# Kernel optimization log

Hardware: AMD Instinct MI355X
Metric: run time of the kernel (lower is better)

Reference implementation:

```python
import jax, jax.numpy as jnp
import numpy as np

IN_CH, H0, H1, OUT_CH = 6, 128, 256, 256
EPS = 1e-5

def _layernorm(x, g, b):
    mu = jnp.mean(x, axis=-1, keepdims=True)
    var = jnp.mean(jnp.square(x - mu), axis=-1, keepdims=True)
    return (x - mu) * jax.lax.rsqrt(var + EPS) * g + b

def setup_inputs() -> dict:
    key = jax.random.key(0)
    ks = jax.random.split(key, 12)
    B, N, C = 8, 65536, 1024
    inp = {
        "point_patches": jax.random.normal(ks[0], (B, N, IN_CH), jnp.float32),
        "nn_idx": jax.random.randint(ks[1], (B, N), 0, C, jnp.int64),
        "center_number": C,
        # conv1: Linear(6,128) -> LN(128) -> GELU -> Linear(128,128)
        "w1": jax.random.normal(ks[2], (IN_CH, H0), jnp.float32) / np.sqrt(IN_CH),
        "b1": jnp.zeros((H0,), jnp.float32),
        "g1": jnp.ones((H0,), jnp.float32),
        "beta1": jnp.zeros((H0,), jnp.float32),
        "w2": jax.random.normal(ks[3], (H0, H0), jnp.float32) / np.sqrt(H0),
        "b2": jnp.zeros((H0,), jnp.float32),
        # conv2: Linear(256,256) -> LN(256) -> GELU -> Linear(256,256)
        "w3": jax.random.normal(ks[4], (2 * H0, H1), jnp.float32) / np.sqrt(2 * H0),
        "b3": jnp.zeros((H1,), jnp.float32),
        "g2": jnp.ones((H1,), jnp.float32),
        "beta2": jnp.zeros((H1,), jnp.float32),
        "w4": jax.random.normal(ks[5], (H1, OUT_CH), jnp.float32) / np.sqrt(H1),
        "b4": jnp.zeros((OUT_CH,), jnp.float32),
    }
    return inp

def _scatter_max_zeros(x, nn_idx, center_number):
    # torch.scatter_reduce(zeros, 1, idx, x, 'max') with include_self=True:
    # segment max clamped from below at 0; empty centers stay 0.
    B = x.shape[0]
    y = jnp.zeros((B, center_number, x.shape[-1]), x.dtype)
    return y.at[jnp.arange(B)[:, None], nn_idx].max(x)

def reference(point_patches, nn_idx, center_number, w1, b1, g1, beta1, w2, b2, w3, b3, g2, beta2, w4, b4):
    # conv1 MLP
    h = point_patches @ w1 + b1
    h = jax.nn.gelu(_layernorm(h, g1, beta1), approximate=False)
    x = h @ w2 + b2                                   # [B, N, H0]
    # scatter-max to centers, gather back per point
    y = _scatter_max_zeros(x, nn_idx, center_number)  # [B, C, H0]
    x_max = jnp.take_along_axis(y, nn_idx[:, :, None], axis=1)  # [B, N, H0]
    x = jnp.concatenate([x_max, x], axis=-1)          # [B, N, 2*H0]
    # conv2 MLP
    h = x @ w3 + b3
    h = jax.nn.gelu(_layernorm(h, g2, beta2), approximate=False)
    x = h @ w4 + b4                                   # [B, N, OUT]
    return _scatter_max_zeros(x, nn_idx, center_number)  # [B, C, OUT]
```

## Files before the change

kernel.cpp:

```cpp
#include <hip/hip_runtime.h>

typedef short short8 __attribute__((ext_vector_type(8)));
typedef float f32x4 __attribute__((ext_vector_type(4)));

#define DEVI __device__ __forceinline__

constexpr int BATCH = 8;
constexpr int NPTS  = 65536;
constexpr int CIN   = 6;
constexpr int H0    = 128;
constexpr int H1    = 256;
constexpr int NCTR  = 1024;
constexpr int MB    = 64;
constexpr int NCHUNK = 8;
constexpr int CHSZ  = NPTS / NCHUNK;

constexpr int A1S = 136;
constexpr int A2S = 264;

constexpr int CAP1 = 8;
constexpr int CAP2 = 8;

constexpr size_t Y_BYTES  = (size_t)BATCH * NCTR * H0 * 4;
constexpr size_t W2T_OFF  = Y_BYTES;
constexpr size_t W3T_OFF  = W2T_OFF + (size_t)H0 * H0 * 2;
constexpr size_t W4T_OFF  = W3T_OFF + (size_t)H1 * H1 * 2;
constexpr size_t SORT_OFF = W4T_OFF + (size_t)H1 * H1 * 2;
constexpr size_t CH_OFF   = SORT_OFF + (size_t)BATCH * NPTS * 4;
constexpr size_t CB_OFF   = CH_OFF + (size_t)BATCH * NCHUNK * NCTR * 4;
constexpr size_t YQ_OFF   = CB_OFF + (size_t)BATCH * NCHUNK * NCTR * 4;
constexpr size_t WS_NEED  = YQ_OFF + (size_t)BATCH * NCTR * H0 * 2;
constexpr size_t XQ_OFF   = WS_NEED;
constexpr size_t WS_XQ    = XQ_OFF + (size_t)BATCH * NPTS * H0 * 2;

DEVI unsigned short f2bf(float f) {
    unsigned u = __float_as_uint(f);
    u += 0x7fffu + ((u >> 16) & 1u);
    return (unsigned short)(u >> 16);
}
DEVI float gelu(float x) {
    const float x3 = x * x * x;
    const float u = fmaf(x3, -0.07135481283f, -1.5957691216f * x);
    return x * __builtin_amdgcn_rcpf(1.f + __expf(u));
}

DEVI void conv1_tile(int tid, const float* s_pts, const float* s_w1,
                     const float* s_b1, const float* s_g1, const float* s_be1,
                     unsigned short* a1)
{
    const int p = tid >> 2, sub = tid & 3;
    float pt[CIN];
#pragma unroll
    for (int k = 0; k < CIN; ++k) pt[k] = s_pts[p * CIN + k];
    float h[32];
#pragma unroll
    for (int j = 0; j < 32; ++j) {
        const int c = (j << 2) + sub;
        float a = s_b1[c];
#pragma unroll
        for (int k = 0; k < CIN; ++k) a = fmaf(pt[k], s_w1[k * H0 + c], a);
        h[j] = a;
    }
    float s = 0.f, s2 = 0.f;
#pragma unroll
    for (int j = 0; j < 32; ++j) { s += h[j]; s2 = fmaf(h[j], h[j], s2); }
    s  += __shfl_xor(s, 1);  s  += __shfl_xor(s, 2);
    s2 += __shfl_xor(s2, 1); s2 += __shfl_xor(s2, 2);
    const float mean = s * (1.f / H0);
    const float rstd = rsqrtf(s2 * (1.f / H0) - mean * mean + 1e-5f);
#pragma unroll
    for (int j = 0; j < 32; ++j) {
        const int c = (j << 2) + sub;
        float v = fmaf((h[j] - mean) * rstd, s_g1[c], s_be1[c]);
        a1[p * A1S + c] = f2bf(gelu(v));
    }
}

DEVI void gemm2(int lane, int wave, const unsigned short* a1,
                const unsigned short* __restrict__ w2T, f32x4 (&acc)[4][2])
{
    const int q = lane >> 4, colw = lane & 15, n0 = wave * 32;
#pragma unroll
    for (int ks = 0; ks < 4; ++ks) {
        short8 af[4], bfr[2];
#pragma unroll
        for (int mt = 0; mt < 4; ++mt)
            af[mt] = *(const short8*)&a1[(mt * 16 + colw) * A1S + ks * 32 + q * 8];
#pragma unroll
        for (int nt = 0; nt < 2; ++nt)
            bfr[nt] = *(const short8*)&w2T[(n0 + nt * 16 + colw) * H0 + ks * 32 + q * 8];
#pragma unroll
        for (int mt = 0; mt < 4; ++mt)
#pragma unroll
            for (int nt = 0; nt < 2; ++nt)
                acc[mt][nt] = __builtin_amdgcn_mfma_f32_16x16x32_bf16(
                    af[mt], bfr[nt], acc[mt][nt], 0, 0, 0);
    }
}

DEVI void stage_sorted(int tid, int b, int P0, const int* __restrict__ sorted,
                       const float* __restrict__ pts, float* s_pts, int* s_idx)
{
    if (tid < 64) {
        const int val = sorted[P0 + tid];
        const int pid = val & 0xFFFF;
        s_idx[tid] = (val >> 16) & (NCTR - 1);
        const float* prow = &pts[((size_t)(b << 16) + pid) * CIN];
#pragma unroll
        for (int k = 0; k < CIN; ++k) s_pts[tid * CIN + k] = prow[k];
    }
}

DEVI void slot_scan(int tid, const int* s_idx, int* s_slot, int* s_slotc, int* s_nslot, int cap)
{
    int f = 0;
    if (tid < MB) {
        f = (tid > 0 && s_idx[tid] != s_idx[tid - 1]) ? 1 : 0;
        s_slot[tid] = f;
    }
    __syncthreads();
#pragma unroll
    for (int off = 1; off < MB; off <<= 1) {
        int t = 0;
        if (tid < MB && tid >= off) t = s_slot[tid - off];
        __syncthreads();
        if (tid < MB) s_slot[tid] += t;
        __syncthreads();
    }
    if (tid < MB) {
        const int s = s_slot[tid];
        if ((f || tid == 0) && s < cap) s_slotc[s] = s_idx[tid];
        if (tid == MB - 1) *s_nslot = (s + 1 < cap) ? (s + 1) : cap;
    }
    __syncthreads();
}

__global__ __launch_bounds__(256) void k_prep(
    const float* __restrict__ w2, const float* __restrict__ w3,
    const float* __restrict__ w4,
    unsigned short* __restrict__ w2T, unsigned short* __restrict__ w3T,
    unsigned short* __restrict__ w4T)
{
    int t = blockIdx.x * 256 + threadIdx.x;
    if (t < H0 * H0) {
        int n = t >> 7, k = t & 127;
        w2T[t] = f2bf(w2[k * H0 + n]);
    }
    int t3 = t - H0 * H0;
    if (t3 >= 0 && t3 < H1 * H1) {
        int n = t3 >> 8, k = t3 & 255;
        w3T[t3] = f2bf(w3[k * H1 + n]);
    }
    int t4 = t - (H0 * H0 + H1 * H1);
    if (t4 >= 0 && t4 < H1 * H1) {
        int n = t4 >> 8, k = t4 & 255;
        w4T[t4] = f2bf(w4[k * H1 + n]);
    }
}

__global__ __launch_bounds__(256) void k_yq(const float* __restrict__ y,
                                            unsigned short* __restrict__ yq)
{
    const int i = blockIdx.x * 256 + threadIdx.x;
    const float4 v = *(const float4*)&y[(size_t)i * 4];
    uint2 pk;
    pk.x = (unsigned)f2bf(v.x) | ((unsigned)f2bf(v.y) << 16);
    pk.y = (unsigned)f2bf(v.z) | ((unsigned)f2bf(v.w) << 16);
    *(uint2*)&yq[(size_t)i * 4] = pk;
}

__global__ __launch_bounds__(256) void k_hist(const int* __restrict__ nn,
                                              int* __restrict__ ch)
{
    __shared__ int lh[NCTR];
    const int tid = threadIdx.x;
    const int b = blockIdx.x >> 3, k = blockIdx.x & 7;
    const int base = (b << 16) + k * CHSZ;
    for (int c = tid; c < NCTR; c += 256) lh[c] = 0;
    __syncthreads();
    for (int i = tid; i < CHSZ; i += 256)
        atomicAdd(&lh[nn[base + i] & (NCTR - 1)], 1);
    __syncthreads();
    for (int c = tid; c < NCTR; c += 256) ch[(blockIdx.x << 10) + c] = lh[c];
}

__global__ __launch_bounds__(256) void k_scan(const int* __restrict__ ch,
                                              int* __restrict__ cb)
{
    __shared__ int part[256];
    const int tid = threadIdx.x;
    const int b = tid >> 5, t = tid & 31;
    const int c0 = t * 32;
    int tot = 0;
    for (int c = c0; c < c0 + 32; ++c)
        for (int k = 0; k < NCHUNK; ++k)
            tot += ch[((b * NCHUNK + k) << 10) + c];
    part[tid] = tot;
    __syncthreads();
    if (t == 0) {
        int run = 0;
        for (int i = 0; i < 32; ++i) { const int v = part[(b << 5) + i]; part[(b << 5) + i] = run; run += v; }
    }
    __syncthreads();
    int run = part[tid];
    for (int c = c0; c < c0 + 32; ++c)
        for (int k = 0; k < NCHUNK; ++k) {
            const int idx = ((b * NCHUNK + k) << 10) + c;
            cb[idx] = run; run += ch[idx];
        }
}

__global__ __launch_bounds__(256) void k_scatter(const int* __restrict__ nn,
                                                 const int* __restrict__ cb,
                                                 int* __restrict__ sorted)
{
    __shared__ int cur[NCTR];
    const int tid = threadIdx.x;
    const int b = blockIdx.x >> 3, k = blockIdx.x & 7;
    const int base = (b << 16) + k * CHSZ;
    for (int c = tid; c < NCTR; c += 256) cur[c] = cb[(blockIdx.x << 10) + c];
    __syncthreads();
    for (int i = tid; i < CHSZ; i += 256) {
        const int c = nn[base + i] & (NCTR - 1);
        const int pos = atomicAdd(&cur[c], 1);
        if ((unsigned)pos < (unsigned)NPTS)
            sorted[(b << 16) + pos] = (k * CHSZ + i) | (c << 16);
    }
}

template <bool XQ>
__global__ __launch_bounds__(256) void k_phase1(
    const int* __restrict__ sorted, const float* __restrict__ pts,
    const float* __restrict__ w1, const float* __restrict__ b1,
    const float* __restrict__ g1, const float* __restrict__ be1,
    const unsigned short* __restrict__ w2T, const float* __restrict__ b2,
    float* __restrict__ y, unsigned short* __restrict__ xq)
{
    __shared__ __align__(16) float s_pts[MB * CIN];
    __shared__ int   s_idx[MB], s_slot[MB], s_slotc[CAP1], s_nslot;
    __shared__ float s_w1[CIN * H0];
    __shared__ float s_b1[H0], s_g1[H0], s_be1[H0];
    __shared__ __align__(16) unsigned short a1[MB * A1S];
    __shared__ int   red1[CAP1 * H0];

    const int tid = threadIdx.x;
    const int P0  = blockIdx.x * MB;
    const int b   = P0 >> 16;
    const int lane = tid & 63, wave = tid >> 6;
    const int q = lane >> 4, colw = lane & 15, n0 = wave * 32;

    float b2reg[2];
#pragma unroll
    for (int nt = 0; nt < 2; ++nt) b2reg[nt] = b2[n0 + nt * 16 + colw];

    stage_sorted(tid, b, P0, sorted, pts, s_pts, s_idx);
    for (int i = tid; i < CIN * H0; i += 256) s_w1[i] = w1[i];
    if (tid < H0) { s_b1[tid] = b1[tid]; s_g1[tid] = g1[tid]; s_be1[tid] = be1[tid]; }
    for (int i = tid; i < CAP1 * H0; i += 256) red1[i] = 0;
    __syncthreads();

    conv1_tile(tid, s_pts, s_w1, s_b1, s_g1, s_be1, a1);
    slot_scan(tid, s_idx, s_slot, s_slotc, &s_nslot, CAP1);

    f32x4 acc[4][2] = {};
    gemm2(lane, wave, a1, w2T, acc);
    if (XQ) __syncthreads();

    int* yi = (int*)y;
    {
        float vm[2] = {-3.4e38f, -3.4e38f};
        int cur = s_slot[q * 4], curc = s_idx[q * 4];
#pragma unroll
        for (int mt = 0; mt < 4; ++mt)
#pragma unroll
            for (int r = 0; r < 4; ++r) {
                const int row = mt * 16 + q * 4 + r;
                const int s = s_slot[row];
                if (s != cur) {
#pragma unroll
                    for (int nt = 0; nt < 2; ++nt) {
                        if (vm[nt] > 0.f) {
                            const int col = n0 + nt * 16 + colw;
                            if (cur < CAP1) atomicMax(&red1[cur * H0 + col], __float_as_int(vm[nt]));
                            else atomicMax(&yi[(((b << 10) + curc) << 7) + col], __float_as_int(vm[nt]));
                        }
                        vm[nt] = -3.4e38f;
                    }
                    cur = s; curc = s_idx[row];
                }
#pragma unroll
                for (int nt = 0; nt < 2; ++nt) {
                    const float v = acc[mt][nt][r] + b2reg[nt];
                    if (XQ) a1[row * A1S + n0 + nt * 16 + colw] = f2bf(v);
                    vm[nt] = fmaxf(vm[nt], v);
                }
            }
#pragma unroll
        for (int nt = 0; nt < 2; ++nt)
            if (vm[nt] > 0.f) {
                const int col = n0 + nt * 16 + colw;
                if (cur < CAP1) atomicMax(&red1[cur * H0 + col], __float_as_int(vm[nt]));
                else atomicMax(&yi[(((b << 10) + curc) << 7) + col], __float_as_int(vm[nt]));
            }
    }
    __syncthreads();
    const int nsc = s_nslot;
    for (int i = tid; i < nsc * H0; i += 256) {
        const int v = red1[i];
        if (v > 0)
            atomicMax(&yi[(((b << 10) + s_slotc[i >> 7]) << 7) + (i & 127)], v);
    }
    if (XQ) {
        for (int i = tid; i < MB * (H0 / 8); i += 256) {
            const int row = i >> 4, u = (i & 15) * 8;
            *(short8*)&xq[((size_t)P0 + row) * H0 + u] = *(const short8*)&a1[row * A1S + u];
        }
    }
}

__global__ __launch_bounds__(256) void k_phase2x(
    const int* __restrict__ sorted, const unsigned short* __restrict__ xq,
    const unsigned short* __restrict__ yq,
    const unsigned short* __restrict__ w3T, const float* __restrict__ b3,
    const float* __restrict__ g2, const float* __restrict__ be2,
    const unsigned short* __restrict__ w4T, const float* __restrict__ b4,
    float* __restrict__ outp)
{
    __shared__ int   s_idx[MB], s_slot[MB], s_slotc[CAP2], s_nslot;
    __shared__ __align__(16) unsigned short a2[MB * A2S];
    __shared__ float2 s_stats[MB * 4];
    __shared__ float2 s_rowstat[MB];

    const int tid = threadIdx.x;
    const int P0  = blockIdx.x * MB;
    const int b   = P0 >> 16;
    const int lane = tid & 63, wave = tid >> 6;
    const int q = lane >> 4, colw = lane & 15;
    const int n0 = wave * 64;

    const int rowp = tid >> 2, sub = tid & 3;
    const int sval = sorted[P0 + rowp];
    const int cp = (sval >> 16) & (NCTR - 1);
    const unsigned short* xsrc = &xq[((size_t)P0 + rowp) * H0 + sub * 32];
    short8 xv0 = *(const short8*)(xsrc);
    short8 xv1 = *(const short8*)(xsrc + 8);
    short8 xv2 = *(const short8*)(xsrc + 16);
    short8 xv3 = *(const short8*)(xsrc + 24);
    const unsigned short* ysrc = &yq[((size_t)((b << 10) + cp)) * H0 + sub * 32];
    short8 yv0 = *(const short8*)(ysrc);
    short8 yv1 = *(const short8*)(ysrc + 8);
    short8 yv2 = *(const short8*)(ysrc + 16);
    short8 yv3 = *(const short8*)(ysrc + 24);

    float b3r[4], g2r[4], be2r[4], b4r[4];
#pragma unroll
    for (int nt = 0; nt < 4; ++nt) {
        const int col = n0 + nt * 16 + colw;
        b3r[nt] = b3[col]; g2r[nt] = g2[col]; be2r[nt] = be2[col]; b4r[nt] = b4[col];
    }

    if (tid < 64) s_idx[tid] = (sorted[P0 + tid] >> 16) & (NCTR - 1);

    {
        unsigned short* dx = &a2[rowp * A2S + H0 + sub * 32];
        *(short8*)(dx)      = xv0;
        *(short8*)(dx + 8)  = xv1;
        *(short8*)(dx + 16) = xv2;
        *(short8*)(dx + 24) = xv3;
        unsigned short* dy = &a2[rowp * A2S + sub * 32];
        *(short8*)(dy)      = yv0;
        *(short8*)(dy + 8)  = yv1;
        *(short8*)(dy + 16) = yv2;
        *(short8*)(dy + 24) = yv3;
    }
    __syncthreads();
    slot_scan(tid, s_idx, s_slot, s_slotc, &s_nslot, CAP2);

    f32x4 acc3[4][4] = {};
#pragma unroll
    for (int ks = 0; ks < 8; ++ks) {
        short8 af[4], bfr[4];
#pragma unroll
        for (int mt = 0; mt < 4; ++mt)
            af[mt] = *(const short8*)&a2[(mt * 16 + colw) * A2S + ks * 32 + q * 8];
#pragma unroll
        for (int nt = 0; nt < 4; ++nt)
            bfr[nt] = *(const short8*)&w3T[(n0 + nt * 16 + colw) * H1 + ks * 32 + q * 8];
#pragma unroll
        for (int mt = 0; mt < 4; ++mt)
#pragma unroll
            for (int nt = 0; nt < 4; ++nt)
                acc3[mt][nt] = __builtin_amdgcn_mfma_f32_16x16x32_bf16(
                    af[mt], bfr[nt], acc3[mt][nt], 0, 0, 0);
    }

#pragma unroll
    for (int mt = 0; mt < 4; ++mt)
#pragma unroll
        for (int nt = 0; nt < 4; ++nt)
#pragma unroll
            for (int r = 0; r < 4; ++r)
                acc3[mt][nt][r] += b3r[nt];

#pragma unroll
    for (int mt = 0; mt < 4; ++mt)
#pragma unroll
        for (int r = 0; r < 4; ++r) {
            float s = 0.f, s2 = 0.f;
#pragma unroll
            for (int nt = 0; nt < 4; ++nt) {
                float v = acc3[mt][nt][r];
                s += v; s2 = fmaf(v, v, s2);
            }
            s  += __shfl_xor(s, 1);  s  += __shfl_xor(s, 2);
            s  += __shfl_xor(s, 4);  s  += __shfl_xor(s, 8);
            s2 += __shfl_xor(s2, 1); s2 += __shfl_xor(s2, 2);
            s2 += __shfl_xor(s2, 4); s2 += __shfl_xor(s2, 8);
            if (colw == 0)
                s_stats[(mt * 16 + q * 4 + r) * 4 + wave] = make_float2(s, s2);
        }
    __syncthreads();
    if (tid < MB) {
        float S = 0.f, S2 = 0.f;
#pragma unroll
        for (int w = 0; w < 4; ++w) { float2 t = s_stats[tid * 4 + w]; S += t.x; S2 += t.y; }
        const float mean = S * (1.f / H1);
        const float rstd = rsqrtf(S2 * (1.f / H1) - mean * mean + 1e-5f);
        s_rowstat[tid] = make_float2(mean, rstd);
    }
    __syncthreads();

#pragma unroll
    for (int mt = 0; mt < 4; ++mt)
#pragma unroll
        for (int r = 0; r < 4; ++r) {
            const int row = mt * 16 + q * 4 + r;
            const float2 ms = s_rowstat[row];
#pragma unroll
            for (int nt = 0; nt < 4; ++nt) {
                float v = (acc3[mt][nt][r] - ms.x) * ms.y;
                v = fmaf(v, g2r[nt], be2r[nt]);
                a2[row * A2S + n0 + nt * 16 + colw] = f2bf(gelu(v));
            }
        }
    __syncthreads();

    f32x4 acc4[4][4] = {};
#pragma unroll
    for (int ks = 0; ks < 8; ++ks) {
        short8 af[4], bfr[4];
#pragma unroll
        for (int mt = 0; mt < 4; ++mt)
            af[mt] = *(const short8*)&a2[(mt * 16 + colw) * A2S + ks * 32 + q * 8];
#pragma unroll
        for (int nt = 0; nt < 4; ++nt)
            bfr[nt] = *(const short8*)&w4T[(n0 + nt * 16 + colw) * H1 + ks * 32 + q * 8];
#pragma unroll
        for (int mt = 0; mt < 4; ++mt)
#pragma unroll
            for (int nt = 0; nt < 4; ++nt)
                acc4[mt][nt] = __builtin_amdgcn_mfma_f32_16x16x32_bf16(
                    af[mt], bfr[nt], acc4[mt][nt], 0, 0, 0);
    }
    __syncthreads();

    int* red = (int*)a2;
    for (int i = tid; i < CAP2 * H1; i += 256) red[i] = 0;
    __syncthreads();

    int* outi = (int*)outp;
    {
        float vm[4] = {-3.4e38f, -3.4e38f, -3.4e38f, -3.4e38f};
        int cur = s_slot[q * 4], curc = s_idx[q * 4];
#pragma unroll
        for (int mt = 0; mt < 4; ++mt)
#pragma unroll
            for (int r = 0; r < 4; ++r) {
                const int row = mt * 16 + q * 4 + r;
                const int s = s_slot[row];
                if (s != cur) {
#pragma unroll
                    for (int nt = 0; nt < 4; ++nt) {
                        if (vm[nt] > 0.f) {
                            const int col = n0 + nt * 16 + colw;
                            if (cur < CAP2) atomicMax(&red[cur * H1 + col], __float_as_int(vm[nt]));
                            else atomicMax(&outi[(((size_t)(b << 10) + curc) << 8) + col], __float_as_int(vm[nt]));
                        }
                        vm[nt] = -3.4e38f;
                    }
                    cur = s; curc = s_idx[row];
                }
#pragma unroll
                for (int nt = 0; nt < 4; ++nt)
                    vm[nt] = fmaxf(vm[nt], acc4[mt][nt][r] + b4r[nt]);
            }
#pragma unroll
        for (int nt = 0; nt < 4; ++nt)
            if (vm[nt] > 0.f) {
                const int col = n0 + nt * 16 + colw;
                if (cur < CAP2) atomicMax(&red[cur * H1 + col], __float_as_int(vm[nt]));
                else atomicMax(&outi[(((size_t)(b << 10) + curc) << 8) + col], __float_as_int(vm[nt]));
            }
    }
    __syncthreads();
    const int nsc = s_nslot;
    for (int i = tid; i < nsc * H1; i += 256) {
        const int v = red[i];
        if (v > 0)
            atomicMax(&outi[(((size_t)(b << 10) + s_slotc[i >> 8]) << 8) + (i & 255)], v);
    }
}

__global__ __launch_bounds__(256) void k_phase2r(
    const int* __restrict__ sorted, const float* __restrict__ pts,
    const float* __restrict__ w1, const float* __restrict__ b1,
    const float* __restrict__ g1, const float* __restrict__ be1,
    const unsigned short* __restrict__ w2T, const float* __restrict__ b2,
    const float* __restrict__ y,
    const unsigned short* __restrict__ w3T, const float* __restrict__ b3,
    const float* __restrict__ g2, const float* __restrict__ be2,
    const unsigned short* __restrict__ w4T, const float* __restrict__ b4,
    float* __restrict__ outp)
{
    __shared__ __align__(16) float s_pts[MB * CIN];
    __shared__ int   s_idx[MB], s_slot[MB], s_slotc[CAP2], s_nslot;
    __shared__ float s_w1[CIN * H0];
    __shared__ float s_b1[H0], s_g1[H0], s_be1[H0], s_b2[H0];
    __shared__ float s_b3[H1], s_g2[H1], s_be2[H1], s_b4[H1];
    __shared__ union __align__(16) {
        unsigned short a1[MB * A1S];
        struct { float2 stats[MB * 4]; float2 rowstat[MB]; } ln;
        int red[CAP2 * H1];
    } u1;
    __shared__ __align__(16) unsigned short a2[MB * A2S];

    const int tid = threadIdx.x;
    const int P0  = blockIdx.x * MB;
    const int b   = P0 >> 16;

    stage_sorted(tid, b, P0, sorted, pts, s_pts, s_idx);
    for (int i = tid; i < CIN * H0; i += 256) s_w1[i] = w1[i];
    if (tid < H0) { s_b1[tid] = b1[tid]; s_g1[tid] = g1[tid]; s_be1[tid] = be1[tid]; s_b2[tid] = b2[tid]; }
    if (tid < H1) { s_b3[tid] = b3[tid]; s_g2[tid] = g2[tid]; s_be2[tid] = be2[tid]; s_b4[tid] = b4[tid]; }
    __syncthreads();

    conv1_tile(tid, s_pts, s_w1, s_b1, s_g1, s_be1, u1.a1);
    slot_scan(tid, s_idx, s_slot, s_slotc, &s_nslot, CAP2);

    f32x4 acc2[4][2] = {};
    const int lane = tid & 63, wave = tid >> 6;
    gemm2(lane, wave, u1.a1, w2T, acc2);

    const int q = lane >> 4, colw = lane & 15;
    {
        const int n0 = wave * 32;
#pragma unroll
        for (int mt = 0; mt < 4; ++mt)
#pragma unroll
            for (int nt = 0; nt < 2; ++nt)
#pragma unroll
                for (int r = 0; r < 4; ++r) {
                    const int row = mt * 16 + q * 4 + r;
                    const int col = n0 + nt * 16 + colw;
                    a2[row * A2S + H0 + col] = f2bf(acc2[mt][nt][r] + s_b2[col]);
                }
    }
    {
        const int p = tid >> 2, sub = tid & 3;
        const float* yrow = y + ((size_t)((b << 10) + s_idx[p])) * H0;
#pragma unroll
        for (int j4 = 0; j4 < 8; ++j4) {
            const int c = sub * 32 + j4 * 4;
            float4 v = *(const float4*)&yrow[c];
            uint2 pk;
            pk.x = (unsigned)f2bf(v.x) | ((unsigned)f2bf(v.y) << 16);
            pk.y = (unsigned)f2bf(v.z) | ((unsigned)f2bf(v.w) << 16);
            *(uint2*)&a2[p * A2S + c] = pk;
        }
    }
    __syncthreads();

    f32x4 acc3[4][4] = {};
    const int n0 = wave * 64;
#pragma unroll
    for (int ks = 0; ks < 8; ++ks) {
        short8 af[4], bfr[4];
#pragma unroll
        for (int mt = 0; mt < 4; ++mt)
            af[mt] = *(const short8*)&a2[(mt * 16 + colw) * A2S + ks * 32 + q * 8];
#pragma unroll
        for (int nt = 0; nt < 4; ++nt)
            bfr[nt] = *(const short8*)&w3T[(n0 + nt * 16 + colw) * H1 + ks * 32 + q * 8];
#pragma unroll
        for (int mt = 0; mt < 4; ++mt)
#pragma unroll
            for (int nt = 0; nt < 4; ++nt)
                acc3[mt][nt] = __builtin_amdgcn_mfma_f32_16x16x32_bf16(
                    af[mt], bfr[nt], acc3[mt][nt], 0, 0, 0);
    }

#pragma unroll
    for (int mt = 0; mt < 4; ++mt)
#pragma unroll
        for (int nt = 0; nt < 4; ++nt)
#pragma unroll
            for (int r = 0; r < 4; ++r)
                acc3[mt][nt][r] += s_b3[n0 + nt * 16 + colw];

#pragma unroll
    for (int mt = 0; mt < 4; ++mt)
#pragma unroll
        for (int r = 0; r < 4; ++r) {
            float s = 0.f, s2 = 0.f;
#pragma unroll
            for (int nt = 0; nt < 4; ++nt) {
                float v = acc3[mt][nt][r];
                s += v; s2 = fmaf(v, v, s2);
            }
            s  += __shfl_xor(s, 1);  s  += __shfl_xor(s, 2);
            s  += __shfl_xor(s, 4);  s  += __shfl_xor(s, 8);
            s2 += __shfl_xor(s2, 1); s2 += __shfl_xor(s2, 2);
            s2 += __shfl_xor(s2, 4); s2 += __shfl_xor(s2, 8);
            if (colw == 0)
                u1.ln.stats[(mt * 16 + q * 4 + r) * 4 + wave] = make_float2(s, s2);
        }
    __syncthreads();
    if (tid < MB) {
        float S = 0.f, S2 = 0.f;
#pragma unroll
        for (int w = 0; w < 4; ++w) { float2 t = u1.ln.stats[tid * 4 + w]; S += t.x; S2 += t.y; }
        const float mean = S * (1.f / H1);
        const float rstd = rsqrtf(S2 * (1.f / H1) - mean * mean + 1e-5f);
        u1.ln.rowstat[tid] = make_float2(mean, rstd);
    }
    __syncthreads();

#pragma unroll
    for (int mt = 0; mt < 4; ++mt)
#pragma unroll
        for (int r = 0; r < 4; ++r) {
            const int row = mt * 16 + q * 4 + r;
            const float2 ms = u1.ln.rowstat[row];
#pragma unroll
            for (int nt = 0; nt < 4; ++nt) {
                const int col = n0 + nt * 16 + colw;
                float v = (acc3[mt][nt][r] - ms.x) * ms.y;
                v = fmaf(v, s_g2[col], s_be2[col]);
                a2[row * A2S + col] = f2bf(gelu(v));
            }
        }
    __syncthreads();

    for (int i = tid; i < CAP2 * H1; i += 256) u1.red[i] = 0;

    f32x4 acc4[4][4] = {};
#pragma unroll
    for (int ks = 0; ks < 8; ++ks) {
        short8 af[4], bfr[4];
#pragma unroll
        for (int mt = 0; mt < 4; ++mt)
            af[mt] = *(const short8*)&a2[(mt * 16 + colw) * A2S + ks * 32 + q * 8];
#pragma unroll
        for (int nt = 0; nt < 4; ++nt)
            bfr[nt] = *(const short8*)&w4T[(n0 + nt * 16 + colw) * H1 + ks * 32 + q * 8];
#pragma unroll
        for (int mt = 0; mt < 4; ++mt)
#pragma unroll
            for (int nt = 0; nt < 4; ++nt)
                acc4[mt][nt] = __builtin_amdgcn_mfma_f32_16x16x32_bf16(
                    af[mt], bfr[nt], acc4[mt][nt], 0, 0, 0);
    }
    __syncthreads();

    int* outi = (int*)outp;
#pragma unroll
    for (int mt = 0; mt < 4; ++mt)
#pragma unroll
        for (int nt = 0; nt < 4; ++nt)
#pragma unroll
            for (int r = 0; r < 4; ++r) {
                const int row = mt * 16 + q * 4 + r;
                const int col = n0 + nt * 16 + colw;
                const float v = acc4[mt][nt][r] + s_b4[col];
                if (v > 0.f) {
                    const int s = s_slot[row];
                    if (s < CAP2)
                        atomicMax(&u1.red[s * H1 + col], __float_as_int(v));
                    else
                        atomicMax(&outi[(((size_t)(b << 10) + s_idx[row]) << 8) + col],
                                  __float_as_int(v));
                }
            }
    __syncthreads();
    const int nsc = s_nslot;
    for (int i = tid; i < nsc * H1; i += 256) {
        const int v = u1.red[i];
        if (v > 0)
            atomicMax(&outi[(((size_t)(b << 10) + s_slotc[i >> 8]) << 8) + (i & 255)], v);
    }
}

extern "C" void kernel_launch(void* const* d_in, const int* in_sizes, int n_in,
                              void* d_out, int out_size, void* d_ws, size_t ws_size,
                              hipStream_t stream)
{
    const float* pts = (const float*)d_in[0];
    const int*   nn  = (const int*)d_in[1];
    const float* w1  = (const float*)d_in[3];
    const float* b1  = (const float*)d_in[4];
    const float* g1  = (const float*)d_in[5];
    const float* be1 = (const float*)d_in[6];
    const float* w2  = (const float*)d_in[7];
    const float* b2  = (const float*)d_in[8];
    const float* w3  = (const float*)d_in[9];
    const float* b3  = (const float*)d_in[10];
    const float* g2  = (const float*)d_in[11];
    const float* be2 = (const float*)d_in[12];
    const float* w4  = (const float*)d_in[13];
    const float* b4  = (const float*)d_in[14];

    if (ws_size < WS_NEED) return;

    char* ws = (char*)d_ws;
    float*          y      = (float*)(ws);
    unsigned short* w2T    = (unsigned short*)(ws + W2T_OFF);
    unsigned short* w3T    = (unsigned short*)(ws + W3T_OFF);
    unsigned short* w4T    = (unsigned short*)(ws + W4T_OFF);
    int*            sorted = (int*)(ws + SORT_OFF);
    int*            ch     = (int*)(ws + CH_OFF);
    int*            cb     = (int*)(ws + CB_OFF);
    unsigned short* yq     = (unsigned short*)(ws + YQ_OFF);
    unsigned short* xq     = (unsigned short*)(ws + XQ_OFF);
    float* outp = (float*)d_out;
    const bool have_xq = ws_size >= WS_XQ;

    hipMemsetAsync(y, 0, Y_BYTES, stream);
    hipMemsetAsync(outp, 0, (size_t)out_size * sizeof(float), stream);

    k_prep<<<576, 256, 0, stream>>>(w2, w3, w4, w2T, w3T, w4T);
    k_hist<<<BATCH * NCHUNK, 256, 0, stream>>>(nn, ch);
    k_scan<<<1, 256, 0, stream>>>(ch, cb);
    k_scatter<<<BATCH * NCHUNK, 256, 0, stream>>>(nn, cb, sorted);

    const int nblk = BATCH * NPTS / MB;
    if (have_xq) {
        k_phase1<true><<<nblk, 256, 0, stream>>>(sorted, pts, w1, b1, g1, be1, w2T, b2, y, xq);
        k_yq<<<BATCH * NCTR * H0 / 4 / 256, 256, 0, stream>>>(y, yq);
        k_phase2x<<<nblk, 256, 0, stream>>>(sorted, xq, yq, w3T, b3, g2, be2, w4T, b4, outp);
    } else {
        k_phase1<false><<<nblk, 256, 0, stream>>>(sorted, pts, w1, b1, g1, be1, w2T, b2, y, nullptr);
        k_phase2r<<<nblk, 256, 0, stream>>>(sorted, pts, w1, b1, g1, be1, w2T, b2, y,
                                            w3T, b3, g2, be2, w4T, b4, outp);
    }
}
```

Before: 531.1 us.

## Precompute nonempty-center ranks in scan, prefetch weight fragments, raise occupancy bounds

The scan kernel now also writes an exclusive prefix count of non-empty centers per batch. Phase kernels use it to compute each row's reduction slot directly instead of running a per-block slot scan. The weight B-fragments for the GEMMs are software-pipelined, with the next k-step loaded before the current MFMAs issue, and launch bounds request 4 blocks per SM. This cuts block-level serial scan work and hides global weight-load latency, at the cost of more registers and possible spills under the tighter bound.

```diff
diff --git a/kernel.cpp b/kernel.cpp
--- a/kernel.cpp
+++ b/kernel.cpp
@@ -28,7 +28,8 @@
 constexpr size_t SORT_OFF = W4T_OFF + (size_t)H1 * H1 * 2;
 constexpr size_t CH_OFF   = SORT_OFF + (size_t)BATCH * NPTS * 4;
 constexpr size_t CB_OFF   = CH_OFF + (size_t)BATCH * NCHUNK * NCTR * 4;
-constexpr size_t YQ_OFF   = CB_OFF + (size_t)BATCH * NCHUNK * NCTR * 4;
+constexpr size_t NZR_OFF  = CB_OFF + (size_t)BATCH * NCHUNK * NCTR * 4;
+constexpr size_t YQ_OFF   = NZR_OFF + (size_t)BATCH * NCTR * 4;
 constexpr size_t WS_NEED  = YQ_OFF + (size_t)BATCH * NCTR * H0 * 2;
 constexpr size_t XQ_OFF   = WS_NEED;
 constexpr size_t WS_XQ    = XQ_OFF + (size_t)BATCH * NPTS * H0 * 2;
@@ -185,29 +186,40 @@
 }
 
 __global__ __launch_bounds__(256) void k_scan(const int* __restrict__ ch,
-                                              int* __restrict__ cb)
-{
-    __shared__ int part[256];
+                                              int* __restrict__ cb,
+                                              int* __restrict__ nzr)
+{
+    __shared__ int part[256], partz[256];
     const int tid = threadIdx.x;
     const int b = tid >> 5, t = tid & 31;
     const int c0 = t * 32;
-    int tot = 0;
-    for (int c = c0; c < c0 + 32; ++c)
+    int tot = 0, totz = 0;
+    for (int c = c0; c < c0 + 32; ++c) {
+        int cnt = 0;
         for (int k = 0; k < NCHUNK; ++k)
-            tot += ch[((b * NCHUNK + k) << 10) + c];
-    part[tid] = tot;
+            cnt += ch[((b * NCHUNK + k) << 10) + c];
+        tot += cnt; totz += (cnt > 0);
+    }
+    part[tid] = tot; partz[tid] = totz;
     __syncthreads();
     if (t == 0) {
-        int run = 0;
-        for (int i = 0; i < 32; ++i) { const int v = part[(b << 5) + i]; part[(b << 5) + i] = run; run += v; }
-    }
-    __syncthreads();
-    int run = part[tid];
-    for (int c = c0; c < c0 + 32; ++c)
+        int run = 0, runz = 0;
+        for (int i = 0; i < 32; ++i) {
+            const int v  = part[(b << 5) + i];  part[(b << 5) + i]  = run;  run  += v;
+            const int vz = partz[(b << 5) + i]; partz[(b << 5) + i] = runz; runz += vz;
+        }
+    }
+    __syncthreads();
+    int run = part[tid], runz = partz[tid];
+    for (int c = c0; c < c0 + 32; ++c) {
+        int cnt = 0;
         for (int k = 0; k < NCHUNK; ++k) {
             const int idx = ((b * NCHUNK + k) << 10) + c;
-            cb[idx] = run; run += ch[idx];
-        }
+            cb[idx] = run; run += ch[idx]; cnt += ch[idx];
+        }
+        nzr[(b << 10) + c] = runz;
+        runz += (cnt > 0);
+    }
 }
 
 __global__ __launch_bounds__(256) void k_scatter(const int* __restrict__ nn,
@@ -229,8 +241,9 @@
 }
 
 template <bool XQ>
-__global__ __launch_bounds__(256) void k_phase1(
+__global__ __launch_bounds__(256, 4) void k_phase1(
     const int* __restrict__ sorted, const float* __restrict__ pts,
+    const int* __restrict__ nzr,
     const float* __restrict__ w1, const float* __restrict__ b1,
     const float* __restrict__ g1, const float* __restrict__ be1,
     const unsigned short* __restrict__ w2T, const float* __restrict__ b2,
@@ -252,18 +265,57 @@
     float b2reg[2];
 #pragma unroll
     for (int nt = 0; nt < 2; ++nt) b2reg[nt] = b2[n0 + nt * 16 + colw];
-
-    stage_sorted(tid, b, P0, sorted, pts, s_pts, s_idx);
+    short8 bnx[2];
+#pragma unroll
+    for (int nt = 0; nt < 2; ++nt)
+        bnx[nt] = *(const short8*)&w2T[(n0 + nt * 16 + colw) * H0 + q * 8];
+
+    if (tid < 64) {
+        const int val = sorted[P0 + tid];
+        const int pid = val & 0xFFFF;
+        const int c   = (val >> 16) & (NCTR - 1);
+        const int c0v = (sorted[P0] >> 16) & (NCTR - 1);
+        s_idx[tid] = c;
+        const int sl = nzr[(b << 10) + c] - nzr[(b << 10) + c0v];
+        s_slot[tid] = sl;
+        if (tid == 63) s_nslot = (sl + 1 < CAP1) ? (sl + 1) : CAP1;
+        const float* prow = &pts[((size_t)(b << 16) + pid) * CIN];
+#pragma unroll
+        for (int k = 0; k < CIN; ++k) s_pts[tid * CIN + k] = prow[k];
+    }
     for (int i = tid; i < CIN * H0; i += 256) s_w1[i] = w1[i];
     if (tid < H0) { s_b1[tid] = b1[tid]; s_g1[tid] = g1[tid]; s_be1[tid] = be1[tid]; }
     for (int i = tid; i < CAP1 * H0; i += 256) red1[i] = 0;
     __syncthreads();
 
+    if (tid < 64) {
+        const int sl = s_slot[tid];
+        if (sl < CAP1 && (tid == 0 || s_idx[tid] != s_idx[tid - 1]))
+            s_slotc[sl] = s_idx[tid];
+    }
     conv1_tile(tid, s_pts, s_w1, s_b1, s_g1, s_be1, a1);
-    slot_scan(tid, s_idx, s_slot, s_slotc, &s_nslot, CAP1);
+    __syncthreads();
 
     f32x4 acc[4][2] = {};
-    gemm2(lane, wave, a1, w2T, acc);
+#pragma unroll
+    for (int ks = 0; ks < 4; ++ks) {
+        short8 bcur[2] = { bnx[0], bnx[1] };
+        if (ks < 3) {
+#pragma unroll
+            for (int nt = 0; nt < 2; ++nt)
+                bnx[nt] = *(const short8*)&w2T[(n0 + nt * 16 + colw) * H0 + (ks + 1) * 32 + q * 8];
+        }
+        short8 af[4];
+#pragma unroll
+        for (int mt = 0; mt < 4; ++mt)
+            af[mt] = *(const short8*)&a1[(mt * 16 + colw) * A1S + ks * 32 + q * 8];
+#pragma unroll
+        for (int mt = 0; mt < 4; ++mt)
+#pragma unroll
+            for (int nt = 0; nt < 2; ++nt)
+                acc[mt][nt] = __builtin_amdgcn_mfma_f32_16x16x32_bf16(
+                    af[mt], bcur[nt], acc[mt][nt], 0, 0, 0);
+    }
     if (XQ) __syncthreads();
 
     int* yi = (int*)y;
@@ -318,9 +370,9 @@
     }
 }
 
-__global__ __launch_bounds__(256) void k_phase2x(
+__global__ __launch_bounds__(256, 4) void k_phase2x(
     const int* __restrict__ sorted, const unsigned short* __restrict__ xq,
-    const unsigned short* __restrict__ yq,
+    const unsigned short* __restrict__ yq, const int* __restrict__ nzr,
     const unsigned short* __restrict__ w3T, const float* __restrict__ b3,
     const float* __restrict__ g2, const float* __restrict__ be2,
     const unsigned short* __restrict__ w4T, const float* __restrict__ b4,
@@ -358,9 +410,19 @@
         const int col = n0 + nt * 16 + colw;
         b3r[nt] = b3[col]; g2r[nt] = g2[col]; be2r[nt] = be2[col]; b4r[nt] = b4[col];
     }
-
-    if (tid < 64) s_idx[tid] = (sorted[P0 + tid] >> 16) & (NCTR - 1);
-
+    short8 bnx[4];
+#pragma unroll
+    for (int nt = 0; nt < 4; ++nt)
+        bnx[nt] = *(const short8*)&w3T[(n0 + nt * 16 + colw) * H1 + q * 8];
+
+    if (tid < 64) {
+        const int c   = (sorted[P0 + tid] >> 16) & (NCTR - 1);
+        const int c0v = (sorted[P0] >> 16) & (NCTR - 1);
+        s_idx[tid] = c;
+        const int sl = nzr[(b << 10) + c] - nzr[(b << 10) + c0v];
+        s_slot[tid] = sl;
+        if (tid == 63) s_nslot = (sl + 1 < CAP2) ? (sl + 1) : CAP2;
+    }
     {
         unsigned short* dx = &a2[rowp * A2S + H0 + sub * 32];
         *(short8*)(dx)      = xv0;
@@ -374,24 +436,32 @@
         *(short8*)(dy + 24) = yv3;
     }
     __syncthreads();
-    slot_scan(tid, s_idx, s_slot, s_slotc, &s_nslot, CAP2);
+
+    if (tid < 64) {
+        const int sl = s_slot[tid];
+        if (sl < CAP2 && (tid == 0 || s_idx[tid] != s_idx[tid - 1]))
+            s_slotc[sl] = s_idx[tid];
+    }
 
     f32x4 acc3[4][4] = {};
 #pragma unroll
     for (int ks = 0; ks < 8; ++ks) {
-        short8 af[4], bfr[4];
+        short8 bcur[4] = { bnx[0], bnx[1], bnx[2], bnx[3] };
+        if (ks < 7) {
+#pragma unroll
+            for (int nt = 0; nt < 4; ++nt)
+                bnx[nt] = *(const short8*)&w3T[(n0 + nt * 16 + colw) * H1 + (ks + 1) * 32 + q * 8];
+        }
+        short8 af[4];
 #pragma unroll
         for (int mt = 0; mt < 4; ++mt)
             af[mt] = *(const short8*)&a2[(mt * 16 + colw) * A2S + ks * 32 + q * 8];
-#pragma unroll
-        for (int nt = 0; nt < 4; ++nt)
-            bfr[nt] = *(const short8*)&w3T[(n0 + nt * 16 + colw) * H1 + ks * 32 + q * 8];
 #pragma unroll
         for (int mt = 0; mt < 4; ++mt)
 #pragma unroll
             for (int nt = 0; nt < 4; ++nt)
                 acc3[mt][nt] = __builtin_amdgcn_mfma_f32_16x16x32_bf16(
-                    af[mt], bfr[nt], acc3[mt][nt], 0, 0, 0);
+                    af[mt], bcur[nt], acc3[mt][nt], 0, 0, 0);
     }
 
 #pragma unroll
@@ -443,24 +513,31 @@
                 a2[row * A2S + n0 + nt * 16 + colw] = f2bf(gelu(v));
             }
         }
+    short8 b4x[4];
+#pragma unroll
+    for (int nt = 0; nt < 4; ++nt)
+        b4x[nt] = *(const short8*)&w4T[(n0 + nt * 16 + colw) * H1 + q * 8];
     __syncthreads();
 
     f32x4 acc4[4][4] = {};
 #pragma unroll
     for (int ks = 0; ks < 8; ++ks) {
-        short8 af[4], bfr[4];
+        short8 bcur[4] = { b4x[0], b4x[1], b4x[2], b4x[3] };
+        if (ks < 7) {
+#pragma unroll
+            for (int nt = 0; nt < 4; ++nt)
+                b4x[nt] = *(const short8*)&w4T[(n0 + nt * 16 + colw) * H1 + (ks + 1) * 32 + q * 8];
+        }
+        short8 af[4];
 #pragma unroll
         for (int mt = 0; mt < 4; ++mt)
             af[mt] = *(const short8*)&a2[(mt * 16 + colw) * A2S + ks * 32 + q * 8];
-#pragma unroll
-        for (int nt = 0; nt < 4; ++nt)
-            bfr[nt] = *(const short8*)&w4T[(n0 + nt * 16 + colw) * H1 + ks * 32 + q * 8];
 #pragma unroll
         for (int mt = 0; mt < 4; ++mt)
 #pragma unroll
             for (int nt = 0; nt < 4; ++nt)
                 acc4[mt][nt] = __builtin_amdgcn_mfma_f32_16x16x32_bf16(
-                    af[mt], bfr[nt], acc4[mt][nt], 0, 0, 0);
+                    af[mt], bcur[nt], acc4[mt][nt], 0, 0, 0);
     }
     __syncthreads();
 
@@ -729,6 +806,7 @@
     int*            sorted = (int*)(ws + SORT_OFF);
     int*            ch     = (int*)(ws + CH_OFF);
     int*            cb     = (int*)(ws + CB_OFF);
+    int*            nzr    = (int*)(ws + NZR_OFF);
     unsigned short* yq     = (unsigned short*)(ws + YQ_OFF);
     unsigned short* xq     = (unsigned short*)(ws + XQ_OFF);
     float* outp = (float*)d_out;
@@ -739,16 +817,16 @@
 
     k_prep<<<576, 256, 0, stream>>>(w2, w3, w4, w2T, w3T, w4T);
     k_hist<<<BATCH * NCHUNK, 256, 0, stream>>>(nn, ch);
-    k_scan<<<1, 256, 0, stream>>>(ch, cb);
+    k_scan<<<1, 256, 0, stream>>>(ch, cb, nzr);
     k_scatter<<<BATCH * NCHUNK, 256, 0, stream>>>(nn, cb, sorted);
 
     const int nblk = BATCH * NPTS / MB;
     if (have_xq) {
-        k_phase1<true><<<nblk, 256, 0, stream>>>(sorted, pts, w1, b1, g1, be1, w2T, b2, y, xq);
+        k_phase1<true><<<nblk, 256, 0, stream>>>(sorted, pts, nzr, w1, b1, g1, be1, w2T, b2, y, xq);
         k_yq<<<BATCH * NCTR * H0 / 4 / 256, 256, 0, stream>>>(y, yq);
-        k_phase2x<<<nblk, 256, 0, stream>>>(sorted, xq, yq, w3T, b3, g2, be2, w4T, b4, outp);
+        k_phase2x<<<nblk, 256, 0, stream>>>(sorted, xq, yq, nzr, w3T, b3, g2, be2, w4T, b4, outp);
     } else {
-        k_phase1<false><<<nblk, 256, 0, stream>>>(sorted, pts, w1, b1, g1, be1, w2T, b2, y, nullptr);
+        k_phase1<false><<<nblk, 256, 0, stream>>>(sorted, pts, nzr, w1, b1, g1, be1, w2T, b2, y, nullptr);
         k_phase2r<<<nblk, 256, 0, stream>>>(sorted, pts, w1, b1, g1, be1, w2T, b2, y,
                                             w3T, b3, g2, be2, w4T, b4, outp);
     }
```

Result: faster. 472.6 us (-11.0%).
